# Performance work log

Measured on AMD Instinct MI355X. Metric: run time of the kernel, lower is better.

## Reference

```python
import jax, jax.numpy as jnp
import numpy as np

W = 128; H = 128; NEAR = 0.1; FAR = 10.0; EPS = 1e-8
B = 1; V = 512; F = 1024


def _perspective(cf, cc):
    # OpenGL-convention projection, returned transposed for row-vector multiply
    f = 0.5 * (cf[0] + cf[1]); pco = 0.5
    right = (W - (cc[0] + pco)) * (NEAR / f)
    left = -(cc[0] + pco) * (NEAR / f)
    top = (cc[1] + pco) * (NEAR / f)
    bottom = -(H - cc[1] + pco) * (NEAR / f)
    z = jnp.zeros(())
    m = jnp.stack([
        jnp.stack([2.0 * NEAR / (right - left), z, (right + left) / (right - left), z]),
        jnp.stack([z, 2.0 * NEAR / (top - bottom), (top + bottom) / (top - bottom), z]),
        jnp.stack([z, z, jnp.full((), -(FAR + NEAR) / (FAR - NEAR)), jnp.full((), -2.0 * FAR * NEAR / (FAR - NEAR))]),
        jnp.stack([z, z, jnp.full((), -1.0), z]),
    ])
    return m.T


def _rodrigues(r):
    theta = jnp.sqrt(jnp.sum(r * r) + 1e-12)
    k = r / theta
    zz = jnp.zeros(())
    K = jnp.stack([
        jnp.stack([zz, -k[2], k[1]]),
        jnp.stack([k[2], zz, -k[0]]),
        jnp.stack([-k[1], k[0], zz]),
    ])
    return jnp.eye(3) + jnp.sin(theta) * K + (1.0 - jnp.cos(theta)) * (K @ K)


def _view_matrix(rt, t):
    # row-vector convention: v' = v @ M, M = rodrigues^T composed with translation-in-last-row
    R = _rodrigues(rt)
    Mr = jnp.eye(4).at[:3, :3].set(R.T)
    Mt = jnp.eye(4).at[3, :3].set(t)
    return Mr @ Mt


def _rasterize_one(vs_xy, z_ndc, inv_w, valid_tri, f, vc, bgcolor, px, py):
    # vs_xy [V,2] screen coords, z_ndc [V], inv_w [V]; f [F,3] int; pixels px,py [P]
    a = vs_xy[f[:, 0]]; b = vs_xy[f[:, 1]]; c = vs_xy[f[:, 2]]  # [F,2]
    x = px[:, None]; y = py[:, None]  # [P,1]
    def E(p, q):  # signed edge function, broadcast to [P,F]
        return (q[:, 0] - p[:, 0]) * (y - p[:, 1]) - (q[:, 1] - p[:, 1]) * (x - p[:, 0])
    w0 = E(b, c); w1 = E(c, a); w2 = E(a, b)  # [P,F]
    area = (b[:, 0] - a[:, 0]) * (c[:, 1] - a[:, 1]) - (b[:, 1] - a[:, 1]) * (c[:, 0] - a[:, 0])  # [F]
    area_safe = jnp.where(jnp.abs(area) > EPS, area, 1.0)
    b0 = w0 / area_safe; b1 = w1 / area_safe; b2 = w2 / area_safe
    za = z_ndc[f[:, 0]]; zb = z_ndc[f[:, 1]]; zc = z_ndc[f[:, 2]]
    z = b0 * za + b1 * zb + b2 * zc  # [P,F] interpolated NDC depth
    inside = ((b0 >= 0) & (b1 >= 0) & (b2 >= 0) & (jnp.abs(area) > EPS)
              & valid_tri[None, :] & (z >= -1.0) & (z <= 1.0))
    depth = jnp.where(inside, z, jnp.inf)
    best = jnp.argmin(depth, axis=1)  # [P] z-buffer winner
    covered = jnp.take_along_axis(depth, best[:, None], 1)[:, 0] <= 1.0
    take = lambda m: jnp.take_along_axis(m, best[:, None], 1)[:, 0]
    bs = jnp.stack([take(b0), take(b1), take(b2)], -1)  # [P,3]
    tri = f[best]          # [P,3]
    iw = inv_w[tri]        # [P,3]
    col = vc[tri]          # [P,3,C]
    den = jnp.sum(bs * iw, -1)
    den = jnp.where(jnp.abs(den) > EPS, den, 1.0)
    color = jnp.einsum('pk,pk,pkc->pc', bs, iw, col) / den[:, None]  # perspective-correct
    return jnp.where(covered[:, None], color, bgcolor[None, :])  # [P,C]


def reference(v, vc, f, bgcolor, camera_f, camera_c, camera_t, camera_rt):
    view = _view_matrix(camera_rt, camera_t)
    proj = _perspective(camera_f, camera_c)
    vh = jnp.concatenate([v, jnp.ones_like(v[..., :1])], -1)  # [B,V,4]
    clip = vh @ (view @ proj)                                 # [B,V,4]
    wc = clip[..., 3]
    valid_v = wc > EPS                                        # in front of camera
    w_safe = jnp.where(valid_v, wc, 1.0)
    ndc = clip[..., :3] / w_safe[..., None]
    xs = (ndc[..., 0] * 0.5 + 0.5) * W
    ys = (0.5 - ndc[..., 1] * 0.5) * H
    vs_xy = jnp.stack([xs, ys], -1)                           # [B,V,2]
    inv_w = 1.0 / w_safe
    valid_tri = valid_v[:, f].all(-1)                         # [B,F]
    gy, gx = jnp.meshgrid(jnp.arange(H, dtype=jnp.float32) + 0.5,
                          jnp.arange(W, dtype=jnp.float32) + 0.5, indexing='ij')
    px = gx.reshape(-1); py = gy.reshape(-1)
    img = jax.vmap(lambda xy, zn, iw, vt: _rasterize_one(xy, zn, iw, vt, f, vc, bgcolor, px, py))(
        vs_xy, ndc[..., 2], inv_w, valid_tri)
    return img.reshape(v.shape[0], H, W, vc.shape[-1])


def setup_inputs() -> dict:
    key = jax.random.key(0)
    k1, k2, k3 = jax.random.split(key, 3)
    u = jax.random.uniform(k1, (B, V, 3), dtype=jnp.float32)
    # x,y in [-0.8,0.8], z in [-3,-1] (camera looks along -z)
    vtx = jnp.stack([u[..., 0] * 1.6 - 0.8, u[..., 1] * 1.6 - 0.8, -(1.0 + 2.0 * u[..., 2])], -1)
    vc = jax.random.uniform(k2, (V, 3), dtype=jnp.float32)
    f = jax.random.randint(k3, (F, 3), 0, V, dtype=jnp.int32)
    return {
        'v': vtx,
        'vc': vc,
        'f': f,
        'bgcolor': jnp.zeros((3,), jnp.float32),
        'camera_f': jnp.array([128.0, 128.0], jnp.float32),
        'camera_c': jnp.array([64.0, 64.0], jnp.float32),
        'camera_t': jnp.zeros((3,), jnp.float32),
        'camera_rt': jnp.zeros((3,), jnp.float32),
    }
```

## Files before the change

### kernel.cpp

```cpp
#include <hip/hip_runtime.h>
#include <math.h>
#include <stdint.h>

#define NV 512
#define NF 1024
#define TRI_STRIDE 16
#define TF_STRIDE 20
#define TRI_CHUNK 64
#define NCHUNK (NF / TRI_CHUNK)


__global__ __launch_bounds__(1024) void setup_kernel(
    const float* __restrict__ v, const int* __restrict__ fidx,
    const float* __restrict__ camf, const float* __restrict__ camc,
    const float* __restrict__ camt, const float* __restrict__ camrt,
    double* __restrict__ vdata, double* __restrict__ tridata,
    float* __restrict__ trifast, unsigned long long* __restrict__ keys)
{
#pragma clang fp contract(off)
  __shared__ double sM[16];
  __shared__ double sxs[NV], sys_[NV], szn[NV];
  __shared__ int svld[NV];
  const int tid = threadIdx.x;

  for (int i = tid; i < 16384; i += 1024) keys[i] = ~0ull;

  if (tid == 0) {
    float r0f = camrt[0], r1f = camrt[1], r2f = camrt[2];
    float th = sqrtf(((r0f * r0f + r1f * r1f) + r2f * r2f) + 1e-12f);
    float k0 = r0f / th, k1 = r1f / th, k2 = r2f / th;
    float sthf = sinf(th);
    float cthf = 1.0f - cosf(th);
    double K[3][3] = {{0.0, -(double)k2, (double)k1},
                      {(double)k2, 0.0, -(double)k0},
                      {-(double)k1, (double)k0, 0.0}};
    double KK[3][3];
    for (int i = 0; i < 3; ++i)
      for (int j = 0; j < 3; ++j)
        KK[i][j] = (K[i][0] * K[0][j] + K[i][1] * K[1][j]) + K[i][2] * K[2][j];
    double R[3][3];
    for (int i = 0; i < 3; ++i)
      for (int j = 0; j < 3; ++j) {
        double e = (i == j) ? 1.0 : 0.0;
        R[i][j] = (e + (double)sthf * K[i][j]) + (double)cthf * KK[i][j];
      }
    double Mr[4][4], Mt[4][4];
    for (int i = 0; i < 4; ++i)
      for (int j = 0; j < 4; ++j) {
        Mr[i][j] = (i == j) ? 1.0 : 0.0;
        Mt[i][j] = (i == j) ? 1.0 : 0.0;
      }
    for (int i = 0; i < 3; ++i)
      for (int j = 0; j < 3; ++j) Mr[i][j] = R[j][i];
    Mt[3][0] = (double)camt[0]; Mt[3][1] = (double)camt[1]; Mt[3][2] = (double)camt[2];
    double view[4][4];
    for (int i = 0; i < 4; ++i)
      for (int j = 0; j < 4; ++j)
        view[i][j] = ((Mr[i][0] * Mt[0][j] + Mr[i][1] * Mt[1][j]) +
                      Mr[i][2] * Mt[2][j]) + Mr[i][3] * Mt[3][j];
    float fcam = 0.5f * (camf[0] + camf[1]);
    float nf = 0.1f / fcam;
    float ccx = camc[0], ccy = camc[1];
    float right = (128.0f - (ccx + 0.5f)) * nf;
    float left = -(ccx + 0.5f) * nf;
    float top = (ccy + 0.5f) * nf;
    float bottom = -((128.0f - ccy) + 0.5f) * nf;
    float m00f = 0.2f / (right - left);
    float m02f = (right + left) / (right - left);
    float m11f = 0.2f / (top - bottom);
    float m12f = (top + bottom) / (top - bottom);
    double P[4][4] = {
        {(double)m00f, 0.0, (double)m02f, 0.0},
        {0.0, (double)m11f, (double)m12f, 0.0},
        {0.0, 0.0, -(10.0 + 0.1) / (10.0 - 0.1),
         -2.0 * 10.0 * 0.1 / (10.0 - 0.1)},
        {0.0, 0.0, -1.0, 0.0}};
    for (int i = 0; i < 4; ++i)
      for (int j = 0; j < 4; ++j)
        sM[i * 4 + j] = ((view[i][0] * P[j][0] + view[i][1] * P[j][1]) +
                         view[i][2] * P[j][2]) + view[i][3] * P[j][3];
  }
  __syncthreads();

  if (tid < NV) {
    double x = (double)v[tid * 3 + 0];
    double y = (double)v[tid * 3 + 1];
    double zz = (double)v[tid * 3 + 2];
    double c0 = ((x * sM[0] + y * sM[4]) + zz * sM[8]) + sM[12];
    double c1 = ((x * sM[1] + y * sM[5]) + zz * sM[9]) + sM[13];
    double c2 = ((x * sM[2] + y * sM[6]) + zz * sM[10]) + sM[14];
    double c3 = ((x * sM[3] + y * sM[7]) + zz * sM[11]) + sM[15];
    int valid = c3 > 1e-8;
    double wsafe = valid ? c3 : 1.0;
    double n0 = c0 / wsafe, n1 = c1 / wsafe, n2 = c2 / wsafe;
    double xs = (n0 * 0.5 + 0.5) * 128.0;
    double ys = (0.5 - n1 * 0.5) * 128.0;
    double iw = 1.0 / wsafe;
    sxs[tid] = xs; sys_[tid] = ys; szn[tid] = n2; svld[tid] = valid;
    vdata[0 * NV + tid] = xs;
    vdata[1 * NV + tid] = ys;
    vdata[2 * NV + tid] = n2;
    vdata[3 * NV + tid] = iw;
  }
  __syncthreads();

  {
    int i0 = fidx[tid * 3 + 0], i1 = fidx[tid * 3 + 1], i2 = fidx[tid * 3 + 2];
    double ax = sxs[i0], ay = sys_[i0];
    double bx = sxs[i1], by = sys_[i1];
    double cx = sxs[i2], cy = sys_[i2];
    double p1 = (bx - ax) * (cy - ay);
    double p2 = (by - ay) * (cx - ax);
    double area = p1 - p2;
    bool ok = (fabs(area) > 1e-8) && svld[i0] && svld[i1] && svld[i2];
    double s = (area > 0.0) ? 1.0 : -1.0;
    double inv_abs = ok ? s / area : 1.0;
    double kk0 = szn[i0] * inv_abs, kk1 = szn[i1] * inv_abs, kk2 = szn[i2] * inv_abs;

    double* td = tridata + tid * TRI_STRIDE;
    td[0] = bx;  td[1] = by;  td[2] = cx;  td[3] = cy;  td[4] = ax;  td[5] = ay;
    td[6] = s * (cx - bx);  td[7] = s * (cy - by);
    td[8] = s * (ax - cx);  td[9] = s * (ay - cy);
    td[10] = s * (bx - ax); td[11] = s * (by - ay);
    td[12] = kk0; td[13] = kk1; td[14] = kk2;
    td[15] = inv_abs;

    double e0x = cx - bx, e0y = cy - by;
    double e1x = ax - cx, e1y = ay - cy;
    double e2x = bx - ax, e2y = by - ay;
    double A0 = -s * e0y, B0 = s * e0x, C0 = s * (e0y * bx - e0x * by);
    double A1 = -s * e1y, B1 = s * e1x, C1 = s * (e1y * cx - e1x * cy);
    double A2 = -s * e2y, B2 = s * e2x, C2 = s * (e2y * ax - e2x * ay);
    double Az = (A0 * kk0 + A1 * kk1) + A2 * kk2;
    double Bz = (B0 * kk0 + B1 * kk1) + B2 * kk2;
    double Cz = (C0 * kk0 + C1 * kk1) + C2 * kk2;
    double mag0 = (fabs(A0) + fabs(B0)) * 129.0 + fabs(C0);
    double mag1 = (fabs(A1) + fabs(B1)) * 129.0 + fabs(C1);
    double mag2 = (fabs(A2) + fabs(B2)) * 129.0 + fabs(C2);
    double magw = fmax(mag0, fmax(mag1, mag2));
    double magz = (fabs(Az) + fabs(Bz)) * 129.0 + fabs(Cz);
    double tw = 9.5367431640625e-07 * magw;
    double tz = 9.5367431640625e-07 * magz + 1e-6;
    float bminx, bminy, bmaxx, bmaxy;
    if (ok) {
      bminx = (float)(fmin(fmin(ax, bx), cx) - 0.01);
      bminy = (float)(fmin(fmin(ay, by), cy) - 0.01);
      bmaxx = (float)(fmax(fmax(ax, bx), cx) + 0.01);
      bmaxy = (float)(fmax(fmax(ay, by), cy) + 0.01);
    } else {
      bminx = 1e30f; bminy = 1e30f; bmaxx = -1e30f; bmaxy = -1e30f;
    }
    float* tf = trifast + tid * TF_STRIDE;
    tf[0] = bminx; tf[1] = bminy; tf[2] = bmaxx; tf[3] = bmaxy;
    tf[4] = (float)A0; tf[5] = (float)B0; tf[6] = (float)C0;
    tf[7] = (float)A1; tf[8] = (float)B1; tf[9] = (float)C1;
    tf[10] = (float)A2; tf[11] = (float)B2; tf[12] = (float)C2;
    tf[13] = (float)Az; tf[14] = (float)Bz; tf[15] = (float)Cz;
    tf[16] = (float)tw; tf[17] = (float)tz;
    tf[18] = 0.0f; tf[19] = 0.0f;
  }
}

__global__ __launch_bounds__(256) void raster_kernel(
    const float* __restrict__ trifast, const double* __restrict__ tridata,
    unsigned long long* __restrict__ keys)
{
  const int tid = threadIdx.x;
  const int tile = blockIdx.x;
  const int chunk = blockIdx.y;
  const int x0 = (tile & 7) << 4;
  const int y0 = (tile >> 3) << 4;
  const int x = x0 + (tid & 15);
  const int y = y0 + (tid >> 4);
  const float pxf = (float)x + 0.5f, pyf = (float)y + 0.5f;
  const double px = (double)x + 0.5, py = (double)y + 0.5;
  const float txmin = (float)x0 + 0.5f, txmax = (float)x0 + 15.5f;
  const float tymin = (float)y0 + 0.5f, tymax = (float)y0 + 15.5f;

  double bestz = INFINITY;
  float bestzf = INFINITY;
  int besti = -1;

  const int tbase = chunk * TRI_CHUNK;
  for (int t = 0; t < TRI_CHUNK; ++t) {
    const int tt = __builtin_amdgcn_readfirstlane(tbase + t);
    const float4* tq = (const float4*)(trifast + tt * TF_STRIDE);
    float4 q0 = tq[0];
    if (q0.x > txmax || q0.z < txmin || q0.y > tymax || q0.w < tymin) continue;
    float4 q1 = tq[1];
    float4 q2 = tq[2];
    float4 q3 = tq[3];
    float4 q4 = tq[4];
    float w0f = fmaf(q1.x, pxf, fmaf(q1.y, pyf, q1.z));
    float w1f = fmaf(q1.w, pxf, fmaf(q2.x, pyf, q2.y));
    float w2f = fmaf(q2.z, pxf, fmaf(q2.w, pyf, q3.x));
    float zf  = fmaf(q3.y, pxf, fmaf(q3.z, pyf, q3.w));
    float tw = q4.x, tz = q4.y;
    float zub = fminf(bestzf, 1.0f) + tz;
    bool rej = (w0f < -tw) | (w1f < -tw) | (w2f < -tw) |
               (zf > zub) | (zf < -1.0f - tz);
    if (!rej) {
      const double* td = tridata + tt * TRI_STRIDE;
      double w0 = td[6] * (py - td[1]) - td[7] * (px - td[0]);
      double w1 = td[8] * (py - td[3]) - td[9] * (px - td[2]);
      double w2 = td[10] * (py - td[5]) - td[11] * (px - td[4]);
      double z = (w0 * td[12] + w1 * td[13]) + w2 * td[14];
      bool ins = (w0 >= 0.0) & (w1 >= 0.0) & (w2 >= 0.0) &
                 (z >= -1.0) & (z <= 1.0) & (z < bestz);
      if (ins) { bestz = z; bestzf = (float)z; besti = tt; }
    }
  }
  if (besti >= 0) {
    unsigned long long zq = (unsigned long long)((bestz + 1.0) * 4503599627370496.0);
    unsigned long long key = (zq << 10) | (unsigned long long)besti;
    atomicMin(&keys[y * 128 + x], key);
  }
}

__global__ __launch_bounds__(256) void color_kernel(
    const unsigned long long* __restrict__ keys,
    const double* __restrict__ vdata, const double* __restrict__ tridata,
    const int* __restrict__ fidx, const float* __restrict__ vc,
    const float* __restrict__ bg, float* __restrict__ out)
{
  const int p = blockIdx.x * 256 + threadIdx.x;
  if (p >= 16384) return;
  const int x = p & 127, y = p >> 7;
  unsigned long long key = keys[p];
  float cr, cg, cb;
  if (key == ~0ull) {
    cr = bg[0]; cg = bg[1]; cb = bg[2];
  } else {
    unsigned int t = (unsigned int)(key & 1023ull);
    const double* td = tridata + t * TRI_STRIDE;
    double px = (double)x + 0.5, py = (double)y + 0.5;
    double w0 = td[6] * (py - td[1]) - td[7] * (px - td[0]);
    double w1 = td[8] * (py - td[3]) - td[9] * (px - td[2]);
    double w2 = td[10] * (py - td[5]) - td[11] * (px - td[4]);
    double inv = td[15];
    double b0 = w0 * inv, b1 = w1 * inv, b2 = w2 * inv;
    int i0 = fidx[t * 3 + 0], i1 = fidx[t * 3 + 1], i2 = fidx[t * 3 + 2];
    double t0 = b0 * vdata[3 * NV + i0];
    double t1 = b1 * vdata[3 * NV + i1];
    double t2 = b2 * vdata[3 * NV + i2];
    double den = (t0 + t1) + t2;
    if (!(fabs(den) > 1e-8)) den = 1.0;
    cr = (float)((((t0 * (double)vc[i0 * 3 + 0] + t1 * (double)vc[i1 * 3 + 0]) +
                   t2 * (double)vc[i2 * 3 + 0])) / den);
    cg = (float)((((t0 * (double)vc[i0 * 3 + 1] + t1 * (double)vc[i1 * 3 + 1]) +
                   t2 * (double)vc[i2 * 3 + 1])) / den);
    cb = (float)((((t0 * (double)vc[i0 * 3 + 2] + t1 * (double)vc[i1 * 3 + 2]) +
                   t2 * (double)vc[i2 * 3 + 2])) / den);
  }
  out[p * 3 + 0] = cr;
  out[p * 3 + 1] = cg;
  out[p * 3 + 2] = cb;
}

extern "C" void kernel_launch(void* const* d_in, const int* in_sizes, int n_in,
                              void* d_out, int out_size, void* d_ws, size_t ws_size,
                              hipStream_t stream) {
  const float* v = (const float*)d_in[0];
  const float* vc = (const float*)d_in[1];
  const int* fidx = (const int*)d_in[2];
  const float* bg = (const float*)d_in[3];
  const float* camf = (const float*)d_in[4];
  const float* camc = (const float*)d_in[5];
  const float* camt = (const float*)d_in[6];
  const float* camrt = (const float*)d_in[7];
  float* out = (float*)d_out;

  char* ws = (char*)d_ws;
  unsigned long long* keys = (unsigned long long*)ws;
  double* vdata = (double*)(ws + 131072);
  double* tridata = (double*)(ws + 147456);
  float* trifast = (float*)(ws + 278528);

  setup_kernel<<<1, 1024, 0, stream>>>(v, fidx, camf, camc, camt, camrt,
                                       vdata, tridata, trifast, keys);
  raster_kernel<<<dim3(64, NCHUNK), 256, 0, stream>>>(trifast, tridata, keys);
  color_kernel<<<64, 256, 0, stream>>>(keys, vdata, tridata, fidx, vc, bg, out);
}
```

Baseline: 105.2 us.

## Stage triangle data in LDS and cut raster grid to fewer, larger groups

```diff
diff --git a/kernel.cpp b/kernel.cpp
--- a/kernel.cpp
+++ b/kernel.cpp
@@ -6,8 +6,9 @@
 #define NF 1024
 #define TRI_STRIDE 16
 #define TF_STRIDE 20
-#define TRI_CHUNK 64
-#define NCHUNK (NF / TRI_CHUNK)
+#define NGROUP 8
+#define GROUP_TRIS (NF / NGROUP)
+#define CHUNK 64
 
 
 __global__ __launch_bounds__(1024) void setup_kernel(
@@ -165,9 +166,11 @@
     const float* __restrict__ trifast, const double* __restrict__ tridata,
     unsigned long long* __restrict__ keys)
 {
+  __shared__ float sf[CHUNK][TF_STRIDE];
+  __shared__ double sd[CHUNK][TRI_STRIDE];
   const int tid = threadIdx.x;
   const int tile = blockIdx.x;
-  const int chunk = blockIdx.y;
+  const int group = blockIdx.y;
   const int x0 = (tile & 7) << 4;
   const int y0 = (tile >> 3) << 4;
   const int x = x0 + (tid & 15);
@@ -181,33 +184,40 @@
   float bestzf = INFINITY;
   int besti = -1;
 
-  const int tbase = chunk * TRI_CHUNK;
-  for (int t = 0; t < TRI_CHUNK; ++t) {
-    const int tt = __builtin_amdgcn_readfirstlane(tbase + t);
-    const float4* tq = (const float4*)(trifast + tt * TF_STRIDE);
-    float4 q0 = tq[0];
-    if (q0.x > txmax || q0.z < txmin || q0.y > tymax || q0.w < tymin) continue;
-    float4 q1 = tq[1];
-    float4 q2 = tq[2];
-    float4 q3 = tq[3];
-    float4 q4 = tq[4];
-    float w0f = fmaf(q1.x, pxf, fmaf(q1.y, pyf, q1.z));
-    float w1f = fmaf(q1.w, pxf, fmaf(q2.x, pyf, q2.y));
-    float w2f = fmaf(q2.z, pxf, fmaf(q2.w, pyf, q3.x));
-    float zf  = fmaf(q3.y, pxf, fmaf(q3.z, pyf, q3.w));
-    float tw = q4.x, tz = q4.y;
-    float zub = fminf(bestzf, 1.0f) + tz;
-    bool rej = (w0f < -tw) | (w1f < -tw) | (w2f < -tw) |
-               (zf > zub) | (zf < -1.0f - tz);
-    if (!rej) {
-      const double* td = tridata + tt * TRI_STRIDE;
-      double w0 = td[6] * (py - td[1]) - td[7] * (px - td[0]);
-      double w1 = td[8] * (py - td[3]) - td[9] * (px - td[2]);
-      double w2 = td[10] * (py - td[5]) - td[11] * (px - td[4]);
-      double z = (w0 * td[12] + w1 * td[13]) + w2 * td[14];
-      bool ins = (w0 >= 0.0) & (w1 >= 0.0) & (w2 >= 0.0) &
-                 (z >= -1.0) & (z <= 1.0) & (z < bestz);
-      if (ins) { bestz = z; bestzf = (float)z; besti = tt; }
+  for (int c = 0; c < GROUP_TRIS / CHUNK; ++c) {
+    const int tbase = group * GROUP_TRIS + c * CHUNK;
+    __syncthreads();
+    for (int i = tid; i < CHUNK * TF_STRIDE; i += 256)
+      ((float*)sf)[i] = trifast[tbase * TF_STRIDE + i];
+    for (int i = tid; i < CHUNK * TRI_STRIDE * 2; i += 256)
+      ((float*)sd)[i] = ((const float*)(tridata + tbase * TRI_STRIDE))[i];
+    __syncthreads();
+
+    for (int t = 0; t < CHUNK; ++t) {
+      float4 q0 = *(const float4*)&sf[t][0];
+      if (q0.x > txmax || q0.z < txmin || q0.y > tymax || q0.w < tymin) continue;
+      float4 q1 = *(const float4*)&sf[t][4];
+      float4 q2 = *(const float4*)&sf[t][8];
+      float4 q3 = *(const float4*)&sf[t][12];
+      float2 q4 = *(const float2*)&sf[t][16];
+      float w0f = fmaf(q1.x, pxf, fmaf(q1.y, pyf, q1.z));
+      float w1f = fmaf(q1.w, pxf, fmaf(q2.x, pyf, q2.y));
+      float w2f = fmaf(q2.z, pxf, fmaf(q2.w, pyf, q3.x));
+      float zf  = fmaf(q3.y, pxf, fmaf(q3.z, pyf, q3.w));
+      float tw = q4.x, tz = q4.y;
+      float zub = fminf(bestzf, 1.0f) + tz;
+      bool rej = (w0f < -tw) | (w1f < -tw) | (w2f < -tw) |
+                 (zf > zub) | (zf < -1.0f - tz);
+      if (!rej) {
+        const double* td = sd[t];
+        double w0 = td[6] * (py - td[1]) - td[7] * (px - td[0]);
+        double w1 = td[8] * (py - td[3]) - td[9] * (px - td[2]);
+        double w2 = td[10] * (py - td[5]) - td[11] * (px - td[4]);
+        double z = (w0 * td[12] + w1 * td[13]) + w2 * td[14];
+        bool ins = (w0 >= 0.0) & (w1 >= 0.0) & (w2 >= 0.0) &
+                   (z >= -1.0) & (z <= 1.0) & (z < bestz);
+        if (ins) { bestz = z; bestzf = (float)z; besti = tbase + t; }
+      }
     }
   }
   if (besti >= 0) {
@@ -278,6 +288,6 @@
 
   setup_kernel<<<1, 1024, 0, stream>>>(v, fidx, camf, camc, camt, camrt,
                                        vdata, tridata, trifast, keys);
-  raster_kernel<<<dim3(64, NCHUNK), 256, 0, stream>>>(trifast, tridata, keys);
+  raster_kernel<<<dim3(64, NGROUP), 256, 0, stream>>>(trifast, tridata, keys);
   color_kernel<<<64, 256, 0, stream>>>(keys, vdata, tridata, fidx, vc, bg, out);
 }
```

After: 115.0 us. +9.3%, slower.
